# Performance work log

Hardware: AMD Instinct MI355X
Metric: run time of the kernel (lower is better)

Reference implementation:

```python
import jax, jax.numpy as jnp
import numpy as np

USER_DIM = 64
ITEM_DIM = 64
HIDDEN = 32
N_USERS = 50000
N_ITEMS = 50000
N_EDGES = 1_600_000


def _xavier_uniform(key, shape):
    fan_in, fan_out = shape[1], shape[0]
    limit = np.sqrt(6.0 / (fan_in + fan_out))
    return jax.random.uniform(key, shape, jnp.float32, -limit, limit)


def setup_inputs() -> dict:
    key = jax.random.key(0)
    k1, k2, k3, k4, k5 = jax.random.split(key, 5)
    user_embeddings = jax.random.normal(k1, (N_USERS, USER_DIM), jnp.float32)
    item_embeddings = jax.random.normal(k2, (N_ITEMS, ITEM_DIM), jnp.float32)
    edge_index = jax.random.randint(k3, (2, N_EDGES), 0, N_USERS, jnp.int64)
    # MLP params: torch Linear weight is [out, in]; xavier_uniform, zero bias
    W1 = _xavier_uniform(k4, (HIDDEN, USER_DIM + ITEM_DIM))
    b1 = jnp.zeros((HIDDEN,), jnp.float32)
    W2 = _xavier_uniform(k5, (1, HIDDEN))
    b2 = jnp.zeros((1,), jnp.float32)
    return {
        "user_embeddings": user_embeddings,
        "item_embeddings": item_embeddings,
        "W1": W1, "b1": b1, "W2": W2, "b2": b2,
        "edge_index": edge_index,
    }


def reference(user_embeddings, item_embeddings, W1, b1, W2, b2, edge_index):
    user_feats = user_embeddings[edge_index[0]]      # [E, user_dim]
    item_feats = item_embeddings[edge_index[1]]      # [E, item_dim]
    edge_feats = jnp.concatenate([user_feats, item_feats], axis=1)  # [E, user_dim+item_dim]
    h = edge_feats @ W1.T + b1                       # [E, 32]
    h = jnp.where(h >= 0, h, 0.2 * h)                # LeakyReLU(0.2)
    logits = h @ W2.T + b2                           # [E, 1]
    return jax.nn.sigmoid(logits).squeeze(-1)        # [E]
```

## Files before the change

kernel.cpp:

```cpp
#include <hip/hip_runtime.h>

typedef unsigned short ushort_t;
typedef __attribute__((ext_vector_type(8))) short short8;
typedef __attribute__((ext_vector_type(4))) float f32x4;
typedef __attribute__((ext_vector_type(2))) _Float16 h2v;
typedef __attribute__((ext_vector_type(4))) _Float16 h4v;

__device__ __forceinline__ ushort_t f2b(float x) {
    unsigned int u = __builtin_bit_cast(unsigned int, x);
    u += 0x7FFFu + ((u >> 16) & 1u);
    return (ushort_t)(u >> 16);
}

__device__ __forceinline__ short8 pack8(const float* __restrict__ p) {
    float4 f0 = *reinterpret_cast<const float4*>(p);
    float4 f1 = *reinterpret_cast<const float4*>(p + 4);
    short8 v;
    v[0] = (short)f2b(f0.x); v[1] = (short)f2b(f0.y);
    v[2] = (short)f2b(f0.z); v[3] = (short)f2b(f0.w);
    v[4] = (short)f2b(f1.x); v[5] = (short)f2b(f1.y);
    v[6] = (short)f2b(f1.z); v[7] = (short)f2b(f1.w);
    return v;
}

__global__ __launch_bounds__(256) void precompute_h(
    const float* __restrict__ ue, const float* __restrict__ ie,
    const float* __restrict__ W1, const float* __restrict__ b1,
    _Float16* __restrict__ hu, _Float16* __restrict__ hi,
    int nu, int ni, int ntu, int ntot)
{
    const int l  = threadIdx.x & 63;
    const int lj = l & 15;
    const int lg = l >> 4;

    int wid = blockIdx.x * (blockDim.x >> 6) + (threadIdx.x >> 6);
    if (wid >= ntot) return;
    const bool isU = wid < ntu;
    const float* tab = isU ? ue : ie;
    _Float16* ht = isU ? hu : hi;
    const int nrows = isU ? nu : ni;
    const int tb   = (isU ? wid : wid - ntu) * 16;
    const int toff = isU ? 0 : 64;

    short8 afrag[2][2];
#pragma unroll
    for (int ks = 0; ks < 2; ++ks)
#pragma unroll
        for (int g = 0; g < 2; ++g)
            afrag[ks][g] = pack8(W1 + (g * 16 + lj) * 128 + toff + ks * 32 + lg * 8);

    int r = tb + lj; if (r >= nrows) r = nrows - 1;
    const float* rp = tab + (long)r * 64;
    short8 bfrag0 = pack8(rp + lg * 8);
    short8 bfrag1 = pack8(rp + 32 + lg * 8);

    f32x4 acc[2];
#pragma unroll
    for (int g = 0; g < 2; ++g)
#pragma unroll
        for (int q = 0; q < 4; ++q)
            acc[g][q] = isU ? b1[g * 16 + lg * 4 + q] : 0.f;

    acc[0] = __builtin_amdgcn_mfma_f32_16x16x32_bf16(afrag[0][0], bfrag0, acc[0], 0, 0, 0);
    acc[1] = __builtin_amdgcn_mfma_f32_16x16x32_bf16(afrag[0][1], bfrag0, acc[1], 0, 0, 0);
    acc[0] = __builtin_amdgcn_mfma_f32_16x16x32_bf16(afrag[1][0], bfrag1, acc[0], 0, 0, 0);
    acc[1] = __builtin_amdgcn_mfma_f32_16x16x32_bf16(afrag[1][1], bfrag1, acc[1], 0, 0, 0);

    if (tb + lj < nrows) {
#pragma unroll
        for (int g = 0; g < 2; ++g) {
            h4v v;
#pragma unroll
            for (int q = 0; q < 4; ++q) v[q] = (_Float16)acc[g][q];
            *reinterpret_cast<h4v*>(ht + (long)r * 32 + g * 16 + lg * 4) = v;
        }
    }
}

#if __has_builtin(__builtin_amdgcn_fdot2)
__device__ __forceinline__ float fdot2(h2v a, h2v b, float c) {
    return __builtin_amdgcn_fdot2(a, b, c, false);
}
#else
__device__ __forceinline__ float fdot2(h2v a, h2v b, float c) {
    return c + (float)a[0] * (float)b[0] + (float)a[1] * (float)b[1];
}
#endif

__global__ __launch_bounds__(256) void edge_final(
    const _Float16* __restrict__ hu, const _Float16* __restrict__ hi,
    const float* __restrict__ w2, const float* __restrict__ b2v,
    const int* __restrict__ idx, float* __restrict__ out,
    long E, long ngroups)
{
    const int l = threadIdx.x & 63;
    const int c = l & 3;
    const int g = l >> 2;

    long wid = (long)blockIdx.x * (blockDim.x >> 6) + (threadIdx.x >> 6);
    if (wid >= ngroups) return;

    h2v w2h[4];
#pragma unroll
    for (int k = 0; k < 4; ++k) {
        w2h[k][0] = (_Float16)w2[c * 8 + 2 * k];
        w2h[k][1] = (_Float16)w2[c * 8 + 2 * k + 1];
    }
    const float bb2 = b2v[0];
    const _Float16 sl = (_Float16)0.2f;
    const h2v slope = {sl, sl};

    long e0 = wid * 64;
    long el = e0 + l; if (el >= E) el = E - 1;
    int uidx = __builtin_nontemporal_load(idx + el);
    int iidx = __builtin_nontemporal_load(idx + E + el);

    uint4 hur[4], hir[4];
#pragma unroll
    for (int s = 0; s < 4; ++s) {
        int u  = __shfl(uidx, s * 16 + g);
        int it = __shfl(iidx, s * 16 + g);
        hur[s] = *reinterpret_cast<const uint4*>(hu + (long)u  * 32 + c * 8);
        hir[s] = *reinterpret_cast<const uint4*>(hi + (long)it * 32 + c * 8);
    }

    float pt[4];
#pragma unroll
    for (int s = 0; s < 4; ++s) {
        const unsigned int* au = reinterpret_cast<const unsigned int*>(&hur[s]);
        const unsigned int* ai = reinterpret_cast<const unsigned int*>(&hir[s]);
        float p = 0.f;
#pragma unroll
        for (int k = 0; k < 4; ++k) {
            h2v a = __builtin_bit_cast(h2v, au[k]);
            h2v b = __builtin_bit_cast(h2v, ai[k]);
            h2v h = a + b;
            h = __builtin_elementwise_max(h, h * slope);
            p = fdot2(h, w2h[k], p);
        }
        p += __shfl_xor(p, 1);
        p += __shfl_xor(p, 2);
        pt[s] = p;
    }

    int src = (l & 15) * 4;
    float v0 = __shfl(pt[0], src);
    float v1 = __shfl(pt[1], src);
    float v2 = __shfl(pt[2], src);
    float v3 = __shfl(pt[3], src);
    int sr = l >> 4;
    float pv = sr == 0 ? v0 : sr == 1 ? v1 : sr == 2 ? v2 : v3;

    float x = pv + bb2;
    float z = __builtin_amdgcn_exp2f(-1.442695040888963f * x);
    float sig = __builtin_amdgcn_rcpf(1.f + z);
    long eo = e0 + l;
    if (eo < E) __builtin_nontemporal_store(sig, out + eo);
}

__global__ __launch_bounds__(256) void edge_mlp_fp32(
    const float* __restrict__ ue, const float* __restrict__ ie,
    const float* __restrict__ W1, const float* __restrict__ b1,
    const float* __restrict__ w2, const float* __restrict__ b2v,
    const int* __restrict__ idx, float* __restrict__ out, long E)
{
    __shared__ float w1s[128][32];
    for (int t = threadIdx.x; t < 4096; t += blockDim.x) {
        int k = t >> 5, j = t & 31;
        w1s[k][j] = W1[j * 128 + k];
    }
    __syncthreads();
    long e = (long)blockIdx.x * blockDim.x + threadIdx.x;
    if (e >= E) return;
    int u = idx[e], it = idx[E + e];
    const float* ur = ue + (long)u * 64;
    const float* ir = ie + (long)it * 64;
    float acc[32];
#pragma unroll
    for (int j = 0; j < 32; ++j) acc[j] = b1[j];
    for (int k = 0; k < 64; k += 4) {
        float4 f = *reinterpret_cast<const float4*>(ur + k);
        float fv[4] = {f.x, f.y, f.z, f.w};
#pragma unroll
        for (int q = 0; q < 4; ++q)
#pragma unroll
            for (int j = 0; j < 32; ++j) acc[j] += w1s[k + q][j] * fv[q];
    }
    for (int k = 0; k < 64; k += 4) {
        float4 f = *reinterpret_cast<const float4*>(ir + k);
        float fv[4] = {f.x, f.y, f.z, f.w};
#pragma unroll
        for (int q = 0; q < 4; ++q)
#pragma unroll
            for (int j = 0; j < 32; ++j) acc[j] += w1s[64 + k + q][j] * fv[q];
    }
    float lgt = b2v[0];
#pragma unroll
    for (int j = 0; j < 32; ++j) {
        float h = acc[j]; h = h >= 0.f ? h : 0.2f * h;
        lgt += h * w2[j];
    }
    out[e] = 1.0f / (1.0f + expf(-lgt));
}

extern "C" void kernel_launch(void* const* d_in, const int* in_sizes, int n_in,
                              void* d_out, int out_size, void* d_ws, size_t ws_size,
                              hipStream_t stream) {
    const float* ue  = (const float*)d_in[0];
    const float* ie  = (const float*)d_in[1];
    const float* W1  = (const float*)d_in[2];
    const float* b1  = (const float*)d_in[3];
    const float* w2  = (const float*)d_in[4];
    const float* b2v = (const float*)d_in[5];
    const int*   idx = (const int*)d_in[6];
    float* out = (float*)d_out;

    long nu = in_sizes[0] / 64;
    long ni = in_sizes[1] / 64;
    long E  = in_sizes[6] / 2;

    size_t need = (size_t)(nu + ni) * 32 * sizeof(_Float16);
    if (ws_size >= need) {
        _Float16* hu = (_Float16*)d_ws;
        _Float16* hi = hu + (size_t)nu * 32;

        int ntu = (int)((nu + 15) / 16);
        int nti = (int)((ni + 15) / 16);
        int ntot = ntu + nti;
        int pblocks = (ntot + 3) / 4;
        precompute_h<<<pblocks, 256, 0, stream>>>(ue, ie, W1, b1, hu, hi,
                                                  (int)nu, (int)ni, ntu, ntot);

        long ngroups = (E + 63) / 64;
        int mblocks = (int)((ngroups + 3) / 4);
        edge_final<<<mblocks, 256, 0, stream>>>(hu, hi, w2, b2v, idx, out, E, ngroups);
    } else {
        edge_mlp_fp32<<<(int)((E + 255) / 256), 256, 0, stream>>>(
            ue, ie, W1, b1, w2, b2v, idx, out, E);
    }
}
```

Before: 44.80 us.

## Bucket edges by index range before gathering projected embeddings

Adds a pass that scatters the edges into 16 buckets keyed by the high bits of the user and item indices, packing each edge's user, item and original position into a 64-bit record. A grid-stride edge kernel then walks the buckets in order and gathers the half-precision hidden projections, so accesses land in a narrower table window and should reuse cache better. In exchange it adds two extra launches, a write and read of an 8-byte record per edge, global atomics, and outputs written back in scattered order. It also needs a workspace of 16*E*8 bytes; if that is not available it falls back to the old path.

Result: slower. 86.09 us (+92.1%).

```diff
diff --git a/kernel.cpp b/kernel.cpp
--- a/kernel.cpp
+++ b/kernel.cpp
@@ -23,6 +23,10 @@
     return v;
 }
 
+__global__ void zero_cursors(unsigned int* __restrict__ c) {
+    if (threadIdx.x < 16) c[threadIdx.x] = 0;
+}
+
 __global__ __launch_bounds__(256) void precompute_h(
     const float* __restrict__ ue, const float* __restrict__ ie,
     const float* __restrict__ W1, const float* __restrict__ b1,
@@ -77,6 +81,38 @@
     }
 }
 
+__global__ __launch_bounds__(1024) void bucket_scatter(
+    const int* __restrict__ idx, unsigned long long* __restrict__ rec,
+    unsigned int* __restrict__ cursors, long E, long cap)
+{
+    __shared__ unsigned int lhist[16];
+    __shared__ unsigned int lbase[16];
+    long e = (long)blockIdx.x * blockDim.x + threadIdx.x;
+    if (threadIdx.x < 16) lhist[threadIdx.x] = 0;
+    __syncthreads();
+    int u = 0, it = 0, b = 0; unsigned int rank = 0;
+    bool valid = e < E;
+    if (valid) {
+        u  = __builtin_nontemporal_load(idx + e);
+        it = __builtin_nontemporal_load(idx + E + e);
+        b  = ((u >> 14) << 2) | (it >> 14);
+        rank = atomicAdd(&lhist[b], 1u);
+    }
+    __syncthreads();
+    if (threadIdx.x < 16) {
+        unsigned int n = lhist[threadIdx.x];
+        lbase[threadIdx.x] = n ? atomicAdd(&cursors[threadIdx.x], n) : 0u;
+    }
+    __syncthreads();
+    if (valid) {
+        long p = (long)b * cap + lbase[b] + rank;
+        unsigned long long r = (unsigned long long)(unsigned)u
+                             | ((unsigned long long)(unsigned)it << 17)
+                             | ((unsigned long long)e << 34);
+        __builtin_nontemporal_store(r, rec + p);
+    }
+}
+
 #if __has_builtin(__builtin_amdgcn_fdot2)
 __device__ __forceinline__ float fdot2(h2v a, h2v b, float c) {
     return __builtin_amdgcn_fdot2(a, b, c, false);
@@ -86,6 +122,89 @@
     return c + (float)a[0] * (float)b[0] + (float)a[1] * (float)b[1];
 }
 #endif
+
+__global__ __launch_bounds__(256) void edge_compute(
+    const _Float16* __restrict__ hu, const _Float16* __restrict__ hi,
+    const unsigned long long* __restrict__ rec, const unsigned int* __restrict__ counts,
+    const float* __restrict__ w2, const float* __restrict__ b2v,
+    float* __restrict__ out, long E, long cap)
+{
+    const int l = threadIdx.x & 63;
+    const int c = l & 3;
+    const int g = l >> 2;
+
+    long cum[17];
+    cum[0] = 0;
+#pragma unroll
+    for (int k = 0; k < 16; ++k) cum[k + 1] = cum[k] + counts[k];
+
+    h2v w2h[4];
+#pragma unroll
+    for (int k = 0; k < 4; ++k) {
+        w2h[k][0] = (_Float16)w2[c * 8 + 2 * k];
+        w2h[k][1] = (_Float16)w2[c * 8 + 2 * k + 1];
+    }
+    const float bb2 = b2v[0];
+    const _Float16 sl = (_Float16)0.2f;
+    const h2v slope = {sl, sl};
+
+    const long nthreads = (long)gridDim.x * blockDim.x;
+    for (long wbase = (long)blockIdx.x * blockDim.x + (long)(threadIdx.x >> 6) * 64;
+         wbase < E; wbase += nthreads) {
+
+        long w = wbase + l;
+        long wc = w < E ? w : E - 1;
+        int b = 0;
+#pragma unroll
+        for (int k = 1; k < 16; ++k) b += (wc >= cum[k]);
+        long p = wc - cum[b];
+        unsigned long long r = __builtin_nontemporal_load(rec + (long)b * cap + p);
+        int u  = (int)(r & 0x1FFFFu);
+        int it = (int)((r >> 17) & 0x1FFFFu);
+        long eo = (long)(r >> 34);
+
+        uint4 hur[4], hir[4];
+#pragma unroll
+        for (int s = 0; s < 4; ++s) {
+            int us  = __shfl(u,  s * 16 + g);
+            int is_ = __shfl(it, s * 16 + g);
+            hur[s] = *reinterpret_cast<const uint4*>(hu + (long)us  * 32 + c * 8);
+            hir[s] = *reinterpret_cast<const uint4*>(hi + (long)is_ * 32 + c * 8);
+        }
+
+        float pt[4];
+#pragma unroll
+        for (int s = 0; s < 4; ++s) {
+            const unsigned int* au = reinterpret_cast<const unsigned int*>(&hur[s]);
+            const unsigned int* ai = reinterpret_cast<const unsigned int*>(&hir[s]);
+            float pp = 0.f;
+#pragma unroll
+            for (int k = 0; k < 4; ++k) {
+                h2v a = __builtin_bit_cast(h2v, au[k]);
+                h2v bb = __builtin_bit_cast(h2v, ai[k]);
+                h2v h = a + bb;
+                h = __builtin_elementwise_max(h, h * slope);
+                pp = fdot2(h, w2h[k], pp);
+            }
+            pp += __shfl_xor(pp, 1);
+            pp += __shfl_xor(pp, 2);
+            pt[s] = pp;
+        }
+
+        int src = (l & 15) * 4;
+        float v0 = __shfl(pt[0], src);
+        float v1 = __shfl(pt[1], src);
+        float v2 = __shfl(pt[2], src);
+        float v3 = __shfl(pt[3], src);
+        int sr = l >> 4;
+        float pv = sr == 0 ? v0 : sr == 1 ? v1 : sr == 2 ? v2 : v3;
+
+        float x = pv + bb2;
+        float z = __builtin_amdgcn_exp2f(-1.442695040888963f * x);
+        float sig = __builtin_amdgcn_rcpf(1.f + z);
+        if (w < E) __builtin_nontemporal_store(sig, out + eo);
+    }
+}
 
 __global__ __launch_bounds__(256) void edge_final(
     const _Float16* __restrict__ hu, const _Float16* __restrict__ hi,
@@ -219,18 +338,33 @@
     long ni = in_sizes[1] / 64;
     long E  = in_sizes[6] / 2;
 
-    size_t need = (size_t)(nu + ni) * 32 * sizeof(_Float16);
-    if (ws_size >= need) {
+    size_t hu_off  = 256;
+    size_t hi_off  = hu_off + (size_t)nu * 64;
+    size_t rec_off = hi_off + (size_t)ni * 64;
+    size_t need_full  = rec_off + (size_t)16 * (size_t)E * 8;
+    size_t need_small = (size_t)(nu + ni) * 64;
+
+    int ntu = (int)((nu + 15) / 16);
+    int nti = (int)((ni + 15) / 16);
+    int ntot = ntu + nti;
+    int pblocks = (ntot + 3) / 4;
+
+    if (ws_size >= need_full && nu <= 65536 && ni <= 65536) {
+        unsigned int* cursors = (unsigned int*)d_ws;
+        _Float16* hu = (_Float16*)((char*)d_ws + hu_off);
+        _Float16* hi = (_Float16*)((char*)d_ws + hi_off);
+        unsigned long long* rec = (unsigned long long*)((char*)d_ws + rec_off);
+
+        zero_cursors<<<1, 64, 0, stream>>>(cursors);
+        bucket_scatter<<<(int)((E + 1023) / 1024), 1024, 0, stream>>>(idx, rec, cursors, E, E);
+        precompute_h<<<pblocks, 256, 0, stream>>>(ue, ie, W1, b1, hu, hi,
+                                                  (int)nu, (int)ni, ntu, ntot);
+        edge_compute<<<768, 256, 0, stream>>>(hu, hi, rec, cursors, w2, b2v, out, E, E);
+    } else if (ws_size >= need_small) {
         _Float16* hu = (_Float16*)d_ws;
         _Float16* hi = hu + (size_t)nu * 32;
-
-        int ntu = (int)((nu + 15) / 16);
-        int nti = (int)((ni + 15) / 16);
-        int ntot = ntu + nti;
-        int pblocks = (ntot + 3) / 4;
         precompute_h<<<pblocks, 256, 0, stream>>>(ue, ie, W1, b1, hu, hi,
                                                   (int)nu, (int)ni, ntu, ntot);
-
         long ngroups = (E + 63) / 64;
         int mblocks = (int)((ngroups + 3) / 4);
         edge_final<<<mblocks, 256, 0, stream>>>(hu, hi, w2, b2v, idx, out, E, ngroups);
```
